# Performance work log

Measured on AMD Instinct MI355X. Metric: run time of the kernel, lower is better.

The kernel has to match this reference:

```python
import jax, jax.numpy as jnp
import numpy as np

B, S, D, H = 4, 1024, 1024, 16
DK = D // H
N_REL = 5


def setup_inputs() -> dict:
    key = jax.random.key(0)
    ks = jax.random.split(key, 16)
    p = lambda k, shape: (jax.random.normal(k, shape, dtype=jnp.float32) * 0.02)
    return {
        "x": jax.random.normal(ks[0], (B, S, D), dtype=jnp.float32),
        "relation_matrix": jax.random.randint(ks[1], (S, S), 0, N_REL, dtype=jnp.int32),
        "mask": jax.random.randint(ks[2], (B, 1, S, S), 0, 2, dtype=jnp.int32),
        "Wq": p(ks[3], (D, D)), "bq": p(ks[4], (D,)),
        "Wk": p(ks[5], (D, D)), "bk": p(ks[6], (D,)),
        "Wv": p(ks[7], (D, D)), "bv": p(ks[8], (D,)),
        "Wo": p(ks[9], (D, D)), "bo": p(ks[10], (D,)),
        "rel_table": p(ks[11], (N_REL, DK)),
        "gamma": jnp.ones((D,), dtype=jnp.float32),
        "beta": jnp.zeros((D,), dtype=jnp.float32),
    }


def reference(x, relation_matrix, mask, Wq, bq, Wk, bk, Wv, bv, Wo, bo, rel_table, gamma, beta):
    b, s = x.shape[0], x.shape[1]
    residual = x
    # projections -> [B, H, S, DK]
    def proj(W, bias):
        return (x @ W + bias).reshape(b, s, H, DK).transpose(0, 2, 1, 3)
    Q, K, V = proj(Wq, bq), proj(Wk, bk), proj(Wv, bv)
    scores = jnp.einsum('bhid,bhjd->bhij', Q, K) / jnp.sqrt(jnp.float32(DK))
    # relation-embedding additive bias: gather [S,S,DK] then contract with Q
    rel_emb = rel_table[relation_matrix]               # [S, S, DK]
    rel_scores = jnp.einsum('bhid,ijd->bhij', Q, rel_emb)
    scores = scores + rel_scores * 0.5
    scores = jnp.where(mask == 0, jnp.float32(-1e9), scores)
    attention = jax.nn.softmax(scores, axis=-1)
    context = jnp.einsum('bhij,bhjd->bhid', attention, V)
    context = context.transpose(0, 2, 1, 3).reshape(b, s, D)
    output = context @ Wo + bo
    # layer norm (eps = 1e-5, torch default)
    y = output + residual
    mu = jnp.mean(y, axis=-1, keepdims=True)
    var = jnp.mean(jnp.square(y - mu), axis=-1, keepdims=True)
    return (y - mu) * jax.lax.rsqrt(var + 1e-5) * gamma + beta
```

## Files before the change

### kernel.cpp

```cpp
#include <hip/hip_runtime.h>
#include <hip/hip_bf16.h>

typedef unsigned short u16;
typedef unsigned int u32;
typedef unsigned char u8;
typedef __attribute__((ext_vector_type(8))) short short8;
typedef __attribute__((ext_vector_type(4))) float f32x4;

__device__ __forceinline__ float b2f(u16 u) {
    union { float f; u32 i; } z; z.i = ((u32)u) << 16; return z.f;
}
__device__ __forceinline__ u16 f2b(float f) {
    union { float f; u32 i; } z; z.f = f;
    u32 i = z.i;
    u32 r = (i + 0x7FFFu + ((i >> 16) & 1u)) >> 16;
    return (u16)r;
}
__device__ __forceinline__ float ldf(const void* p, size_t i, int f) {
    return f ? ((const float*)p)[i] : b2f(((const u16*)p)[i]);
}
__device__ __forceinline__ void gload_lds16(const void* g, void* l) {
    __builtin_amdgcn_global_load_lds(
        (const __attribute__((address_space(1))) u32*)g,
        (__attribute__((address_space(3))) u32*)l,
        16, 0, 0);
}
__device__ __forceinline__ float exp2_hw(float x) {
    float r; asm("v_exp_f32 %0, %1" : "=v"(r) : "v"(x)); return r;
}

struct P14 { const void* p[14]; };
struct S14 { int s[14]; };

__global__ __launch_bounds__(256) void classify_stats(P14 ptrs, S14 szs, int* stats)
{
    __shared__ int   wsm[4], wzr[4], wag[4], way[4], wjk[4];
    __shared__ float wme[4], wmo[4];
    int i = blockIdx.x;
    int t = threadIdx.x, lane = t & 63, w = t >> 6;
    const u16* p16 = (const u16*)ptrs.p[i];
    const u32* p32 = (const u32*)ptrs.p[i];
    int n = szs.s[i];
    int n16 = n < 4096 ? n : 4096;
    int n32 = n16 >> 1;
    int small = 1, zero = 1, allg = 1, anyg = 0, junk = 0;
    float maxe = 0.f, maxo = 0.f;
    for (int k = t; k < n32; k += 256) if (p32[k] >= 8u) small = 0;
    for (int k = t; k < n16; k += 256) {
        u16 ww = p16[k];
        if (ww != 0) zero = 0;
        if (ww == 0x3F80u) anyg = 1;
        else if (ww != 0) allg = 0;
        float a = fabsf(b2f(ww));
        if (k & 1) { if (a < 1e30f && a > maxo) maxo = a; }
        else { if (!(a < 100.0f)) junk++; else if (a > maxe) maxe = a; }
    }
#pragma unroll
    for (int s = 1; s < 64; s <<= 1) {
        small &= __shfl_xor(small, s);
        zero  &= __shfl_xor(zero, s);
        allg  &= __shfl_xor(allg, s);
        anyg  |= __shfl_xor(anyg, s);
        junk  += __shfl_xor(junk, s);
        maxe   = fmaxf(maxe, __shfl_xor(maxe, s));
        maxo   = fmaxf(maxo, __shfl_xor(maxo, s));
    }
    if (lane == 0) { wsm[w]=small; wzr[w]=zero; wag[w]=allg; way[w]=anyg; wjk[w]=junk; wme[w]=maxe; wmo[w]=maxo; }
    __syncthreads();
    if (t == 0) {
        int sm=1,zr=1,ag=1,ay=0,jk=0; float me=0.f,mo=0.f;
        for (int q=0;q<4;++q){ sm&=wsm[q]; zr&=wzr[q]; ag&=wag[q]; ay|=way[q]; jk+=wjk[q]; me=fmaxf(me,wme[q]); mo=fmaxf(mo,wmo[q]); }
        stats[i*8+0]=sm; stats[i*8+1]=zr; stats[i*8+2]=(ag&&ay)?1:0; stats[i*8+3]=jk;
        stats[i*8+4]=__float_as_int(me); stats[i*8+5]=__float_as_int(mo);
    }
}

__global__ __launch_bounds__(64) void classify_bind(S14 szs, const int* stats, int* cls)
{
    if (threadIdx.x != 0) return;
    int xi = -1, mi = -1, ri = -1, rt = -1, gi = -1, bi = -1;
    int wv[4] = {-1,-1,-1,-1}; int nw = 0;
    int bs[4] = {-1,-1,-1,-1}; int nb = 0;
    for (int i = 0; i < 14; ++i) {
        int s = szs.s[i];
        int sm = stats[i*8+0], zr = stats[i*8+1];
        if (s == 4194304) { if (sm) mi = i; else xi = i; }
        else if (s == 1048576) { if (sm) ri = i; else if (nw < 4) wv[nw++] = i; }
        else if (s == 320) rt = i;
        else if (s == 1024) {
            if (zr) bi = i;
            else if (stats[i*8+2]) gi = i;
            else if (nb < 4) bs[nb++] = i;
        }
    }
    bool ok = (xi >= 0) && (mi >= 0) && (ri >= 0) && (rt >= 0) && (gi >= 0) && (bi >= 0)
           && (nw == 4) && (nb == 4);
    if (ok) {
        cls[0] = xi; cls[1] = ri; cls[2] = mi;
        cls[3] = wv[0]; cls[5] = wv[1]; cls[7] = wv[2]; cls[9] = wv[3];
        cls[4] = bs[0]; cls[6] = bs[1]; cls[8] = bs[2]; cls[10] = bs[3];
        cls[11] = rt; cls[12] = gi; cls[13] = bi;
    } else {
        for (int r = 0; r < 14; ++r) cls[r] = r;
    }
    const int froles[12] = {0,3,4,5,6,7,8,9,10,11,12,13};
    for (int r = 0; r < 12; ++r) {
        int role = froles[r]; int idx = cls[role];
        float me = __int_as_float(stats[idx*8+4]);
        float mo = __int_as_float(stats[idx*8+5]);
        cls[16 + role] = (stats[idx*8+3] > 0) || (me == 0.f && mo > 0.f);
    }
    cls[30] = ok ? 1 : 0;
}

__global__ __launch_bounds__(256) void cvt_x_flex(P14 ptrs, const int* cls, u16* xb) {
    const void* x = ptrs.p[cls[0]];
    int f = cls[16];
    int idx = (blockIdx.x * 256 + threadIdx.x) << 2;
    union { u16 u[4]; uint2 v2; } o;
    if (f) {
        float4 v = *(const float4*)((const float*)x + idx);
        o.u[0] = f2b(v.x); o.u[1] = f2b(v.y); o.u[2] = f2b(v.z); o.u[3] = f2b(v.w);
    } else {
        o.v2 = *(const uint2*)((const u16*)x + idx);
    }
    *(uint2*)&xb[idx] = o.v2;
}

__global__ __launch_bounds__(256) void transposeW_flex(P14 ptrs, const int* cls,
                                                       u16* WT3, u16* WoT)
{
    int z = blockIdx.z;
    const void* W = ptrs.p[cls[3 + 2 * z]];
    int f = cls[16 + 3 + 2 * z];
    u16* WT = (z < 3) ? (WT3 + ((size_t)z << 20)) : WoT;
    __shared__ u16 tile[64][72];
    int t = threadIdx.x;
    int n0 = blockIdx.x << 6, k0 = blockIdx.y << 6;
    int r = t >> 2, c = (t & 3) << 4;
    size_t base = (size_t)(k0 + r) * 1024 + n0 + c;
    if (f) {
        const float* src = (const float*)W + base;
#pragma unroll
        for (int x = 0; x < 16; ++x) tile[r][c + x] = f2b(src[x]);
    } else {
        const u16* src = (const u16*)W + base;
#pragma unroll
        for (int x = 0; x < 16; ++x) tile[r][c + x] = src[x];
    }
    __syncthreads();
    union { u16 u[16]; uint4 v[2]; } tmp;
#pragma unroll
    for (int x = 0; x < 16; ++x) tmp.u[x] = tile[c + x][r];
    *(uint4*)&WT[(size_t)(n0 + r) * 1024 + k0 + c]     = tmp.v[0];
    *(uint4*)&WT[(size_t)(n0 + r) * 1024 + k0 + c + 8] = tmp.v[1];
}

__global__ __launch_bounds__(256) void qrel_k(
    const u16* __restrict__ Q, P14 ptrs, const int* cls, float* __restrict__ Qrel)
{
    __shared__ float rt[5][64];
    const void* rel_table = ptrs.p[cls[11]];
    int f9 = cls[16 + 11];
    int t = threadIdx.x;
    for (int p = t; p < 320; p += 256) ((float*)rt)[p] = ldf(rel_table, p, f9);
    __syncthreads();
    int row = blockIdx.x * 256 + t;
    const u16* qrow = Q + ((size_t)row << 6);
    float a0=0.f, a1=0.f, a2=0.f, a3=0.f, a4=0.f;
#pragma unroll
    for (int k8 = 0; k8 < 64; k8 += 8) {
        union { uint4 v; u16 u[8]; } qq;
        qq.v = *(const uint4*)(qrow + k8);
#pragma unroll
        for (int e = 0; e < 8; ++e) {
            float qv = b2f(qq.u[e]);
            a0 += qv * rt[0][k8 + e];
            a1 += qv * rt[1][k8 + e];
            a2 += qv * rt[2][k8 + e];
            a3 += qv * rt[3][k8 + e];
            a4 += qv * rt[4][k8 + e];
        }
    }
    const float S = 0.5f * 1.44269504f;
    float4 o0 = {a0 * S, a1 * S, a2 * S, a3 * S};
    float4 o1 = {a4 * S, -1e9f, -1e9f, -1e9f};
    *(float4*)&Qrel[(size_t)row * 8]     = o0;
    *(float4*)&Qrel[(size_t)row * 8 + 4] = o1;
}

__global__ __launch_bounds__(256) void gemm128_qkv(
    const u16* __restrict__ X, const u16* __restrict__ WT3,
    P14 ptrs, const int* cls,
    u16* __restrict__ Qb, u16* __restrict__ Kb, u16* __restrict__ VTb)
{
    int o = (blockIdx.x & 7) * 192 + (blockIdx.x >> 3);
    int mt = o / 48, rem = o % 48;
    int z = rem >> 4, nt = rem & 15;
    int m0 = mt << 7, n0 = nt << 6;
    const u16* WT = WT3 + ((size_t)z << 20);
    const void* biasp = ptrs.p[cls[4 + 2 * z]];
    int fb = cls[16 + 4 + 2 * z];
    __shared__ u16 As[2][128][4][8];
    __shared__ u16 Bs[2][64][4][8];
    int t = threadIdx.x, lane = t & 63, w = t >> 6;
    int m = lane & 15, quad = lane >> 4;
    int wm = (w >> 1) << 6, wn = (w & 1) << 5;
    int r1 = t >> 2, r2 = 64 + r1, k4 = t & 3;
    const u16* xa  = &X [(size_t)(m0 + r1) * 1024 + k4 * 8];
    const u16* xa2 = &X [(size_t)(m0 + r2) * 1024 + k4 * 8];
    const u16* wb  = &WT[(size_t)(n0 + r1) * 1024 + k4 * 8];
    f32x4 acc[4][2];
#pragma unroll
    for (int i = 0; i < 4; ++i)
#pragma unroll
        for (int j = 0; j < 2; ++j) acc[i][j] = (f32x4){0.f,0.f,0.f,0.f};

    auto stage = [&](int buf, int k0) {
        gload_lds16(xa  + k0, &As[buf][r1][k4][0]);
        gload_lds16(xa2 + k0, &As[buf][r2][k4][0]);
        gload_lds16(wb  + k0, &Bs[buf][r1][k4][0]);
    };
    stage(0, 0);
    stage(1, 32);
    asm volatile("s_waitcnt vmcnt(3)" ::: "memory");
    __builtin_amdgcn_s_barrier();
    __builtin_amdgcn_sched_barrier(0);
    int cur = 0;
    for (int k0 = 0; k0 < 1024; k0 += 32) {
        short8 af[4], bf[2];
#pragma unroll
        for (int mb = 0; mb < 4; ++mb) af[mb] = *(const short8*)&As[cur][wm + mb*16 + m][quad][0];
#pragma unroll
        for (int nb = 0; nb < 2; ++nb) bf[nb] = *(const short8*)&Bs[cur][wn + nb*16 + m][quad][0];
#pragma unroll
        for (int mb = 0; mb < 4; ++mb)
#pragma unroll
            for (int nb = 0; nb < 2; ++nb)
                acc[mb][nb] = __builtin_amdgcn_mfma_f32_16x16x32_bf16(af[mb], bf[nb], acc[mb][nb], 0, 0, 0);
        __builtin_amdgcn_s_barrier();
        __builtin_amdgcn_sched_barrier(0);
        if (k0 + 64 < 1024) {
            stage(cur, k0 + 64);
            asm volatile("s_waitcnt vmcnt(3)" ::: "memory");
        } else {
            asm volatile("s_waitcnt vmcnt(0)" ::: "memory");
        }
        __builtin_amdgcn_s_barrier();
        __builtin_amdgcn_sched_barrier(0);
        cur ^= 1;
    }
    if (z == 2) {
#pragma unroll
        for (int nb = 0; nb < 2; ++nb) {
            int gn = n0 + wn + nb*16 + m;
            int h = gn >> 6, dk = gn & 63;
            float bv = ldf(biasp, gn, fb);
            int sx = (dk & 7) << 3;
#pragma unroll
            for (int mb = 0; mb < 4; ++mb) {
                int gmBase = m0 + wm + mb*16 + (quad << 2);
                int bI = gmBase >> 10, sB = gmBase & 1023;
                int pos = (sB & ~63) | ((sB & 63) ^ sx);
                union { u16 u[4]; uint2 v; } o4;
#pragma unroll
                for (int r = 0; r < 4; ++r) o4.u[r] = f2b(acc[mb][nb][r] + bv);
                *(uint2*)&VTb[((size_t)(bI * 16 + h) << 16) + dk * 1024 + pos] = o4.v;
            }
        }
    } else {
        u16* outp = (z == 0) ? Qb : Kb;
#pragma unroll
        for (int nb = 0; nb < 2; ++nb) {
            int gn = n0 + wn + nb*16 + m;
            int h = gn >> 6, dk = gn & 63;
            float bv = ldf(biasp, gn, fb);
#pragma unroll
            for (int mb = 0; mb < 4; ++mb)
#pragma unroll
                for (int r = 0; r < 4; ++r) {
                    int gm = m0 + wm + mb*16 + (quad << 2) + r;
                    int bI = gm >> 10, s = gm & 1023;
                    int dk2 = (z == 1) ? (dk ^ (((quad * 4 + r) & 7) << 3)) : dk;
                    outp[((size_t)((bI * 16 + h) << 10) + s) * 64 + dk2] = f2b(acc[mb][nb][r] + bv);
                }
        }
    }
}

__global__ __launch_bounds__(256) void gemm_out64(
    const u16* __restrict__ A, const u16* __restrict__ WT,
    P14 ptrs, const int* cls, float* __restrict__ y)
{
    const void* bo   = ptrs.p[cls[10]];
    const void* Xres = ptrs.p[cls[0]];
    int f8 = cls[16 + 10], f0 = cls[16];
    int o = (blockIdx.x & 7) * 128 + (blockIdx.x >> 3);
    int nt = o & 15, mt = o >> 4;
    int n0 = nt << 6, m0 = mt << 6;
    __shared__ u16 As[2][64][4][8];
    __shared__ u16 Bs[2][64][4][8];
    int t = threadIdx.x, lane = t & 63, w = t >> 6;
    int m = lane & 15, quad = lane >> 4;
    int wm = (w >> 1) << 5, wn = (w & 1) << 5;
    int r1 = t >> 2, k4 = t & 3;
    const u16* xa  = &A [(size_t)(m0 + r1) * 1024 + k4 * 8];
    const u16* wb  = &WT[(size_t)(n0 + r1) * 1024 + k4 * 8];
    f32x4 acc[2][2];
#pragma unroll
    for (int i = 0; i < 2; ++i)
#pragma unroll
        for (int j = 0; j < 2; ++j) acc[i][j] = (f32x4){0.f,0.f,0.f,0.f};

    auto stage = [&](int buf, int k0) {
        gload_lds16(xa + k0, &As[buf][r1][k4][0]);
        gload_lds16(wb + k0, &Bs[buf][r1][k4][0]);
    };
    stage(0, 0);
    stage(1, 32);
    asm volatile("s_waitcnt vmcnt(2)" ::: "memory");
    __builtin_amdgcn_s_barrier();
    __builtin_amdgcn_sched_barrier(0);
    int cur = 0;
    for (int k0 = 0; k0 < 1024; k0 += 32) {
        short8 af[2], bf[2];
#pragma unroll
        for (int mb = 0; mb < 2; ++mb) af[mb] = *(const short8*)&As[cur][wm + mb*16 + m][quad][0];
#pragma unroll
        for (int nb = 0; nb < 2; ++nb) bf[nb] = *(const short8*)&Bs[cur][wn + nb*16 + m][quad][0];
#pragma unroll
        for (int mb = 0; mb < 2; ++mb)
#pragma unroll
            for (int nb = 0; nb < 2; ++nb)
                acc[mb][nb] = __builtin_amdgcn_mfma_f32_16x16x32_bf16(af[mb], bf[nb], acc[mb][nb], 0, 0, 0);
        __builtin_amdgcn_s_barrier();
        __builtin_amdgcn_sched_barrier(0);
        if (k0 + 64 < 1024) {
            stage(cur, k0 + 64);
            asm volatile("s_waitcnt vmcnt(2)" ::: "memory");
        } else {
            asm volatile("s_waitcnt vmcnt(0)" ::: "memory");
        }
        __builtin_amdgcn_s_barrier();
        __builtin_amdgcn_sched_barrier(0);
        cur ^= 1;
    }
#pragma unroll
    for (int nb = 0; nb < 2; ++nb) {
        int gn = n0 + wn + nb*16 + m;
        float bb = ldf(bo, gn, f8);
#pragma unroll
        for (int mb = 0; mb < 2; ++mb)
#pragma unroll
            for (int r = 0; r < 4; ++r) {
                int gm = m0 + wm + mb*16 + (quad << 2) + r;
                size_t idx = (size_t)gm * 1024 + gn;
                y[idx] = acc[mb][nb][r] + bb + ldf(Xres, idx, f0);
            }
    }
}

__global__ __launch_bounds__(256) void make_codes(P14 ptrs, const int* cls, u8* codes)
{
    const int* relmat = (const int*)ptrs.p[cls[1]];
    const int* maskp  = (const int*)ptrs.p[cls[2]];
    int bid = blockIdx.x;
    int b = bid >> 8, ti = (bid >> 4) & 15, tj = bid & 15;
    int t = threadIdx.x, lane = t & 63, w = t >> 6;
    int m = lane & 15, quad = lane >> 4;
    const int* mb = maskp + ((size_t)b << 20);
    union { uint4 v; u8 c[16]; } out;
#pragma unroll
    for (int jb = 0; jb < 4; ++jb) {
        int j = tj * 64 + jb * 16 + m;
#pragma unroll
        for (int r = 0; r < 4; ++r) {
            int i = ti * 64 + w * 16 + (quad << 2) + r;
            size_t off = (size_t)i * 1024 + j;
            out.c[jb * 4 + r] = mb[off] ? (u8)relmat[off] : (u8)5;
        }
    }
    ((uint4*)codes)[(size_t)bid * 256 + t] = out.v;
}

__global__ __launch_bounds__(256) void attn_mfma(
    const u16* __restrict__ Q, const u16* __restrict__ K, const u16* __restrict__ VT,
    const float* __restrict__ Qrel, const u8* __restrict__ codes, u16* __restrict__ ctx)
{
    int raw = blockIdx.x;
    int bid = (raw & 7) * 128 + (raw >> 3);
    int bh = bid >> 4, ti = bid & 15;
    int i0 = ti << 6;
    int b = bh >> 4, h = bh & 15;
    const u16* Qp = Q  + ((size_t)bh << 16);
    const u16* Kp = K  + ((size_t)bh << 16);
    const u16* Vp = VT + ((size_t)bh << 16);
    const uint4* ctile = (const uint4*)codes + ((size_t)((b * 16 + ti) * 16) << 8);

    __shared__ u16 Ks[2][64][64];
    __shared__ u16 Vt[64][64];
    __shared__ u16 Pls[64][72];
    __shared__ float Qrl[64][9];

    int t = threadIdx.x, lane = t & 63, w = t >> 6;
    int m = lane & 15, quad = lane >> 4;

    {
        float2 qv = *(const float2*)&Qrel[(((size_t)bh << 10) + i0) * 8 + (t << 1)];
        Qrl[t >> 2][(t & 3) << 1]       = qv.x;
        Qrl[t >> 2][((t & 3) << 1) + 1] = qv.y;
    }

    short8 qfrag0, qfrag1;
    {
        const u16* qr = Qp + (size_t)(i0 + w * 16 + m) * 64 + quad * 8;
        qfrag0 = *(const short8*)qr;
        qfrag1 = *(const short8*)(qr + 32);
    }
    f32x4 O[4];
    float l_part[4];
#pragma unroll
    for (int d = 0; d < 4; ++d) O[d] = (f32x4){0.f,0.f,0.f,0.f};
#pragma unroll
    for (int r = 0; r < 4; ++r) l_part[r] = 0.f;

    int srow = t >> 3, scol8 = (t & 7) << 3;
    const u16* ks0 = Kp + (size_t)srow * 64 + scol8;
    const u16* ks1 = ks0 + 32 * 64;
    const u16* vs0 = Vp + (size_t)srow * 1024 + scol8;
    const u16* vs1 = vs0 + 32 * 1024;

    auto stageK = [&](int buf, int j0) {
        gload_lds16(ks0 + (size_t)j0 * 64, &Ks[buf][srow][scol8]);
        gload_lds16(ks1 + (size_t)j0 * 64, &Ks[buf][srow + 32][scol8]);
    };
    auto stageV = [&](int j0) {
        gload_lds16(vs0 + j0, &Vt[srow][scol8]);
        gload_lds16(vs1 + j0, &Vt[srow + 32][scol8]);
    };

    const float SC = 0.125f * 1.44269504f;
    int kx = (m & 7) << 3;
    u32 paddr = (u32)(uintptr_t)
        ( __attribute__((address_space(3))) u16*)&Pls[w * 16 + (quad << 2)][m];

    stageK(0, 0);
    stageV(0);
    uint4 cN = ctile[t];
    __syncthreads();
    int cur = 0;

    for (int j0 = 0; j0 < 1024; j0 += 64) {
        bool next = (j0 + 64 < 1024);
        if (next) stageK(cur ^ 1, j0 + 64);

        f32x4 acc[4];
#pragma unroll
        for (int jb = 0; jb < 4; ++jb) {
            acc[jb] = (f32x4){0.f,0.f,0.f,0.f};
            short8 kb0 = *(const short8*)&Ks[cur][jb * 16 + m][(quad * 8) ^ kx];
            short8 kb1 = *(const short8*)&Ks[cur][jb * 16 + m][(32 + quad * 8) ^ kx];
            acc[jb] = __builtin_amdgcn_mfma_f32_16x16x32_bf16(qfrag0, kb0, acc[jb], 0, 0, 0);
            acc[jb] = __builtin_amdgcn_mfma_f32_16x16x32_bf16(qfrag1, kb1, acc[jb], 0, 0, 0);
        }
        union { uint4 v; u8 c[16]; } cd;
        cd.v = cN;
        if (next) cN = ctile[(((j0 + 64) >> 6) << 8) + t];

        float sc[4][4];
#pragma unroll
        for (int jb = 0; jb < 4; ++jb) {
#pragma unroll
            for (int r = 0; r < 4; ++r) {
                int il = w * 16 + (quad << 2) + r;
                float p = exp2_hw(acc[jb][r] * SC + Qrl[il][cd.c[jb * 4 + r]]);
                sc[jb][r] = p;
                l_part[r] += p;
            }
        }
#define PWRITE(JB, O0, O1, O2, O3)                                            \
        {                                                                     \
            u32 pk0, pk1;                                                     \
            asm("v_cvt_pk_bf16_f32 %0, %2, %3\n\t"                            \
                "v_cvt_pk_bf16_f32 %1, %4, %5"                                \
                : "=v"(pk0), "=v"(pk1)                                        \
                : "v"(sc[JB][0]), "v"(sc[JB][1]),                             \
                  "v"(sc[JB][2]), "v"(sc[JB][3]));                            \
            asm volatile("ds_write_b16 %0, %1 offset:" O0 "\n\t"              \
                         "ds_write_b16_d16_hi %0, %1 offset:" O1 "\n\t"       \
                         "ds_write_b16 %0, %2 offset:" O2 "\n\t"              \
                         "ds_write_b16_d16_hi %0, %2 offset:" O3              \
                         :: "v"(paddr), "v"(pk0), "v"(pk1) : "memory");       \
        }
        PWRITE(0, "0",  "144", "288", "432")
        PWRITE(1, "32", "176", "320", "464")
        PWRITE(2, "64", "208", "352", "496")
        PWRITE(3, "96", "240", "384", "528")
#undef PWRITE
        asm volatile("s_waitcnt lgkmcnt(0)" ::: "memory");
        __builtin_amdgcn_sched_barrier(0);

        __syncthreads();

        short8 pa0 = *(const short8*)&Pls[w * 16 + m][quad * 8];
        short8 pa1 = *(const short8*)&Pls[w * 16 + m][quad * 8 + 32];
#pragma unroll
        for (int db = 0; db < 4; ++db) {
            short8 vb0 = *(const short8*)&Vt[db * 16 + m][(quad * 8) ^ kx];
            short8 vb1 = *(const short8*)&Vt[db * 16 + m][(32 + quad * 8) ^ kx];
            O[db] = __builtin_amdgcn_mfma_f32_16x16x32_bf16(pa0, vb0, O[db], 0, 0, 0);
            O[db] = __builtin_amdgcn_mfma_f32_16x16x32_bf16(pa1, vb1, O[db], 0, 0, 0);
        }

        __syncthreads();
        if (next) stageV(j0 + 64);
        cur ^= 1;
    }
    float linv[4];
#pragma unroll
    for (int r = 0; r < 4; ++r) {
        float l = l_part[r];
        l += __shfl_xor(l, 1);
        l += __shfl_xor(l, 2);
        l += __shfl_xor(l, 4);
        l += __shfl_xor(l, 8);
        linv[r] = 1.0f / fmaxf(l, 1e-35f);
    }
#pragma unroll
    for (int db = 0; db < 4; ++db)
#pragma unroll
        for (int r = 0; r < 4; ++r) {
            int il = w * 16 + (quad << 2) + r;
            size_t addr = ((size_t)(b * 1024 + i0 + il)) * 1024 + h * 64 + db * 16 + m;
            ctx[addr] = f2b(O[db][r] * linv[r]);
        }
}

__global__ __launch_bounds__(256) void ln_k(
    float* __restrict__ y, P14 ptrs, const int* cls)
{
    const void* gamma = ptrs.p[cls[12]];
    const void* beta  = ptrs.p[cls[13]];
    int f10 = cls[16 + 12], f11 = cls[16 + 13];
    int row = blockIdx.x, t = threadIdx.x;
    float4 v = *(const float4*)&y[(size_t)row * 1024 + (t << 2)];
    float s = v.x + v.y + v.z + v.w;
#pragma unroll
    for (int mm = 1; mm < 64; mm <<= 1) s += __shfl_xor(s, mm);
    __shared__ float sm[8];
    int w = t >> 6, lane = t & 63;
    if (lane == 0) sm[w] = s;
    __syncthreads();
    float mu = (sm[0] + sm[1] + sm[2] + sm[3]) * (1.0f / 1024.0f);
    float dx = v.x - mu, dy = v.y - mu, dz = v.z - mu, dw = v.w - mu;
    float q = dx * dx + dy * dy + dz * dz + dw * dw;
#pragma unroll
    for (int mm = 1; mm < 64; mm <<= 1) q += __shfl_xor(q, mm);
    if (lane == 0) sm[4 + w] = q;
    __syncthreads();
    float var = (sm[4] + sm[5] + sm[6] + sm[7]) * (1.0f / 1024.0f);
    float rs = rsqrtf(var + 1e-5f);
    int c = t << 2;
    float4 o;
    o.x = dx * rs * ldf(gamma, c,     f10) + ldf(beta, c,     f11);
    o.y = dy * rs * ldf(gamma, c + 1, f10) + ldf(beta, c + 1, f11);
    o.z = dz * rs * ldf(gamma, c + 2, f10) + ldf(beta, c + 2, f11);
    o.w = dw * rs * ldf(gamma, c + 3, f10) + ldf(beta, c + 3, f11);
    *(float4*)&y[(size_t)row * 1024 + c] = o;
}

extern "C" void kernel_launch(void* const* d_in, const int* in_sizes, int n_in,
                              void* d_out, int out_size, void* d_ws, size_t ws_size,
                              hipStream_t stream) {
    (void)out_size; (void)ws_size;
    P14 ptrs; S14 szs;
    for (int i = 0; i < 14; ++i) {
        ptrs.p[i] = (i < n_in) ? d_in[i] : d_in[0];
        szs.s[i]  = (i < n_in) ? in_sizes[i] : 0;
    }
    float* out = (float*)d_out;

    char* ws = (char*)d_ws;
    const size_t MB = 1u << 20;
    u16*   WT3   = (u16*)(ws);
    u16*   WoT   = (u16*)(ws + 6 * MB);
    u16*   Xb    = (u16*)(ws + 8 * MB);
    u16*   Qb    = (u16*)(ws + 16 * MB);
    u16*   Kb    = (u16*)(ws + 24 * MB);
    u16*   VTb   = (u16*)(ws + 32 * MB);
    u16*   ctx   = (u16*)(ws + 8 * MB);
    u8*    codes = (u8*)(ws);
    float* Qrel  = (float*)(ws + 4 * MB);
    int*   cls   = (int*)(ws + 40 * MB);
    int*   stats = (int*)(ws + 40 * MB + 512);

    classify_stats<<<14, 256, 0, stream>>>(ptrs, szs, stats);
    classify_bind<<<1, 64, 0, stream>>>(szs, stats, cls);
    cvt_x_flex<<<4096, 256, 0, stream>>>(ptrs, cls, Xb);
    transposeW_flex<<<dim3(16, 16, 4), 256, 0, stream>>>(ptrs, cls, WT3, WoT);
    gemm128_qkv<<<1536, 256, 0, stream>>>(Xb, WT3, ptrs, cls, Qb, Kb, VTb);
    qrel_k<<<256, 256, 0, stream>>>(Qb, ptrs, cls, Qrel);
    make_codes<<<1024, 256, 0, stream>>>(ptrs, cls, codes);
    attn_mfma<<<1024, 256, 0, stream>>>(Qb, Kb, VTb, Qrel, codes, ctx);
    gemm_out64<<<1024, 256, 0, stream>>>(ctx, WoT, ptrs, cls, out);
    ln_k<<<4096, 256, 0, stream>>>(out, ptrs, cls);
}
```

Before: 264.3 us.

## Merge prep and post kernels, replace attention syncthreads with counted vmcnt waits

Fuses the x conversion and weight transpose into one launch, and the mask/relation code builder and Q-relation projection into another, cutting two kernel launches and their tail gaps. In the attention loop, __syncthreads (which drains every outstanding load) is replaced by raw s_barrier plus explicit s_waitcnt vmcnt counts, so the next K tile and code prefetches can stay in flight across barriers. The code prefetch is also moved ahead of the QK MFMAs. The hand-tuned vmcnt counts depend on exactly how many loads each stage issues, so a miscount could silently race.

```diff
diff --git a/kernel.cpp b/kernel.cpp
--- a/kernel.cpp
+++ b/kernel.cpp
@@ -113,80 +113,49 @@
     cls[30] = ok ? 1 : 0;
 }
 
-__global__ __launch_bounds__(256) void cvt_x_flex(P14 ptrs, const int* cls, u16* xb) {
-    const void* x = ptrs.p[cls[0]];
-    int f = cls[16];
-    int idx = (blockIdx.x * 256 + threadIdx.x) << 2;
-    union { u16 u[4]; uint2 v2; } o;
-    if (f) {
-        float4 v = *(const float4*)((const float*)x + idx);
-        o.u[0] = f2b(v.x); o.u[1] = f2b(v.y); o.u[2] = f2b(v.z); o.u[3] = f2b(v.w);
+__global__ __launch_bounds__(256) void prep_k(P14 ptrs, const int* cls,
+                                              u16* xb, u16* WT3, u16* WoT)
+{
+    __shared__ u16 tile[64][72];
+    int bid = blockIdx.x;
+    int t = threadIdx.x;
+    if (bid < 4096) {
+        const void* x = ptrs.p[cls[0]];
+        int f = cls[16];
+        int idx = (bid * 256 + t) << 2;
+        union { u16 u[4]; uint2 v2; } o;
+        if (f) {
+            float4 v = *(const float4*)((const float*)x + idx);
+            o.u[0] = f2b(v.x); o.u[1] = f2b(v.y); o.u[2] = f2b(v.z); o.u[3] = f2b(v.w);
+        } else {
+            o.v2 = *(const uint2*)((const u16*)x + idx);
+        }
+        *(uint2*)&xb[idx] = o.v2;
     } else {
-        o.v2 = *(const uint2*)((const u16*)x + idx);
-    }
-    *(uint2*)&xb[idx] = o.v2;
-}
-
-__global__ __launch_bounds__(256) void transposeW_flex(P14 ptrs, const int* cls,
-                                                       u16* WT3, u16* WoT)
-{
-    int z = blockIdx.z;
-    const void* W = ptrs.p[cls[3 + 2 * z]];
-    int f = cls[16 + 3 + 2 * z];
-    u16* WT = (z < 3) ? (WT3 + ((size_t)z << 20)) : WoT;
-    __shared__ u16 tile[64][72];
-    int t = threadIdx.x;
-    int n0 = blockIdx.x << 6, k0 = blockIdx.y << 6;
-    int r = t >> 2, c = (t & 3) << 4;
-    size_t base = (size_t)(k0 + r) * 1024 + n0 + c;
-    if (f) {
-        const float* src = (const float*)W + base;
-#pragma unroll
-        for (int x = 0; x < 16; ++x) tile[r][c + x] = f2b(src[x]);
-    } else {
-        const u16* src = (const u16*)W + base;
-#pragma unroll
-        for (int x = 0; x < 16; ++x) tile[r][c + x] = src[x];
-    }
-    __syncthreads();
-    union { u16 u[16]; uint4 v[2]; } tmp;
-#pragma unroll
-    for (int x = 0; x < 16; ++x) tmp.u[x] = tile[c + x][r];
-    *(uint4*)&WT[(size_t)(n0 + r) * 1024 + k0 + c]     = tmp.v[0];
-    *(uint4*)&WT[(size_t)(n0 + r) * 1024 + k0 + c + 8] = tmp.v[1];
-}
-
-__global__ __launch_bounds__(256) void qrel_k(
-    const u16* __restrict__ Q, P14 ptrs, const int* cls, float* __restrict__ Qrel)
-{
-    __shared__ float rt[5][64];
-    const void* rel_table = ptrs.p[cls[11]];
-    int f9 = cls[16 + 11];
-    int t = threadIdx.x;
-    for (int p = t; p < 320; p += 256) ((float*)rt)[p] = ldf(rel_table, p, f9);
-    __syncthreads();
-    int row = blockIdx.x * 256 + t;
-    const u16* qrow = Q + ((size_t)row << 6);
-    float a0=0.f, a1=0.f, a2=0.f, a3=0.f, a4=0.f;
-#pragma unroll
-    for (int k8 = 0; k8 < 64; k8 += 8) {
-        union { uint4 v; u16 u[8]; } qq;
-        qq.v = *(const uint4*)(qrow + k8);
-#pragma unroll
-        for (int e = 0; e < 8; ++e) {
-            float qv = b2f(qq.u[e]);
-            a0 += qv * rt[0][k8 + e];
-            a1 += qv * rt[1][k8 + e];
-            a2 += qv * rt[2][k8 + e];
-            a3 += qv * rt[3][k8 + e];
-            a4 += qv * rt[4][k8 + e];
-        }
-    }
-    const float S = 0.5f * 1.44269504f;
-    float4 o0 = {a0 * S, a1 * S, a2 * S, a3 * S};
-    float4 o1 = {a4 * S, -1e9f, -1e9f, -1e9f};
-    *(float4*)&Qrel[(size_t)row * 8]     = o0;
-    *(float4*)&Qrel[(size_t)row * 8 + 4] = o1;
+        int tw = bid - 4096;
+        int bx = tw & 15, by = (tw >> 4) & 15, z = tw >> 8;
+        const void* W = ptrs.p[cls[3 + 2 * z]];
+        int f = cls[16 + 3 + 2 * z];
+        u16* WT = (z < 3) ? (WT3 + ((size_t)z << 20)) : WoT;
+        int n0 = bx << 6, k0 = by << 6;
+        int r = t >> 2, c = (t & 3) << 4;
+        size_t base = (size_t)(k0 + r) * 1024 + n0 + c;
+        if (f) {
+            const float* src = (const float*)W + base;
+#pragma unroll
+            for (int x2 = 0; x2 < 16; ++x2) tile[r][c + x2] = f2b(src[x2]);
+        } else {
+            const u16* src = (const u16*)W + base;
+#pragma unroll
+            for (int x2 = 0; x2 < 16; ++x2) tile[r][c + x2] = src[x2];
+        }
+        __syncthreads();
+        union { u16 u[16]; uint4 v[2]; } tmp;
+#pragma unroll
+        for (int x2 = 0; x2 < 16; ++x2) tmp.u[x2] = tile[c + x2][r];
+        *(uint4*)&WT[(size_t)(n0 + r) * 1024 + k0 + c]     = tmp.v[0];
+        *(uint4*)&WT[(size_t)(n0 + r) * 1024 + k0 + c + 8] = tmp.v[1];
+    }
 }
 
 __global__ __launch_bounds__(256) void gemm128_qkv(
@@ -360,27 +329,59 @@
     }
 }
 
-__global__ __launch_bounds__(256) void make_codes(P14 ptrs, const int* cls, u8* codes)
-{
-    const int* relmat = (const int*)ptrs.p[cls[1]];
-    const int* maskp  = (const int*)ptrs.p[cls[2]];
+__global__ __launch_bounds__(256) void post_k(
+    P14 ptrs, const int* cls, u8* codes, const u16* __restrict__ Q, float* __restrict__ Qrel)
+{
+    __shared__ float rt[5][64];
     int bid = blockIdx.x;
-    int b = bid >> 8, ti = (bid >> 4) & 15, tj = bid & 15;
-    int t = threadIdx.x, lane = t & 63, w = t >> 6;
-    int m = lane & 15, quad = lane >> 4;
-    const int* mb = maskp + ((size_t)b << 20);
-    union { uint4 v; u8 c[16]; } out;
-#pragma unroll
-    for (int jb = 0; jb < 4; ++jb) {
-        int j = tj * 64 + jb * 16 + m;
-#pragma unroll
-        for (int r = 0; r < 4; ++r) {
-            int i = ti * 64 + w * 16 + (quad << 2) + r;
-            size_t off = (size_t)i * 1024 + j;
-            out.c[jb * 4 + r] = mb[off] ? (u8)relmat[off] : (u8)5;
-        }
-    }
-    ((uint4*)codes)[(size_t)bid * 256 + t] = out.v;
+    int t = threadIdx.x;
+    if (bid < 1024) {
+        const int* relmat = (const int*)ptrs.p[cls[1]];
+        const int* maskp  = (const int*)ptrs.p[cls[2]];
+        int b = bid >> 8, ti = (bid >> 4) & 15, tj = bid & 15;
+        int lane = t & 63, w = t >> 6;
+        int m = lane & 15, quad = lane >> 4;
+        const int* mb = maskp + ((size_t)b << 20);
+        union { uint4 v; u8 c[16]; } out;
+#pragma unroll
+        for (int jb = 0; jb < 4; ++jb) {
+            int j = tj * 64 + jb * 16 + m;
+#pragma unroll
+            for (int r = 0; r < 4; ++r) {
+                int i = ti * 64 + w * 16 + (quad << 2) + r;
+                size_t off = (size_t)i * 1024 + j;
+                out.c[jb * 4 + r] = mb[off] ? (u8)relmat[off] : (u8)5;
+            }
+        }
+        ((uint4*)codes)[(size_t)bid * 256 + t] = out.v;
+    } else {
+        const void* rel_table = ptrs.p[cls[11]];
+        int f9 = cls[16 + 11];
+        for (int p = t; p < 320; p += 256) ((float*)rt)[p] = ldf(rel_table, p, f9);
+        __syncthreads();
+        int row = (bid - 1024) * 256 + t;
+        const u16* qrow = Q + ((size_t)row << 6);
+        float a0=0.f, a1=0.f, a2=0.f, a3=0.f, a4=0.f;
+#pragma unroll
+        for (int k8 = 0; k8 < 64; k8 += 8) {
+            union { uint4 v; u16 u[8]; } qq;
+            qq.v = *(const uint4*)(qrow + k8);
+#pragma unroll
+            for (int e = 0; e < 8; ++e) {
+                float qv = b2f(qq.u[e]);
+                a0 += qv * rt[0][k8 + e];
+                a1 += qv * rt[1][k8 + e];
+                a2 += qv * rt[2][k8 + e];
+                a3 += qv * rt[3][k8 + e];
+                a4 += qv * rt[4][k8 + e];
+            }
+        }
+        const float S = 0.5f * 1.44269504f;
+        float4 o0 = {a0 * S, a1 * S, a2 * S, a3 * S};
+        float4 o1 = {a4 * S, -1e9f, -1e9f, -1e9f};
+        *(float4*)&Qrel[(size_t)row * 8]     = o0;
+        *(float4*)&Qrel[(size_t)row * 8 + 4] = o1;
+    }
 }
 
 __global__ __launch_bounds__(256) void attn_mfma(
@@ -452,7 +453,17 @@
 
     for (int j0 = 0; j0 < 1024; j0 += 64) {
         bool next = (j0 + 64 < 1024);
-        if (next) stageK(cur ^ 1, j0 + 64);
+        union { uint4 v; u8 c[16]; } cd;
+        cd.v = cN;
+        if (next) {
+            stageK(cur ^ 1, j0 + 64);
+            cN = ctile[(((j0 + 64) >> 6) << 8) + t];
+            asm volatile("s_waitcnt vmcnt(6)" ::: "memory");
+        } else {
+            asm volatile("s_waitcnt vmcnt(3)" ::: "memory");
+        }
+        __builtin_amdgcn_s_barrier();
+        __builtin_amdgcn_sched_barrier(0);
 
         f32x4 acc[4];
 #pragma unroll
@@ -463,9 +474,6 @@
             acc[jb] = __builtin_amdgcn_mfma_f32_16x16x32_bf16(qfrag0, kb0, acc[jb], 0, 0, 0);
             acc[jb] = __builtin_amdgcn_mfma_f32_16x16x32_bf16(qfrag1, kb1, acc[jb], 0, 0, 0);
         }
-        union { uint4 v; u8 c[16]; } cd;
-        cd.v = cN;
-        if (next) cN = ctile[(((j0 + 64) >> 6) << 8) + t];
 
         float sc[4][4];
 #pragma unroll
@@ -500,7 +508,10 @@
         asm volatile("s_waitcnt lgkmcnt(0)" ::: "memory");
         __builtin_amdgcn_sched_barrier(0);
 
-        __syncthreads();
+        if (next) asm volatile("s_waitcnt vmcnt(3)" ::: "memory");
+        else      asm volatile("s_waitcnt vmcnt(0)" ::: "memory");
+        __builtin_amdgcn_s_barrier();
+        __builtin_amdgcn_sched_barrier(0);
 
         short8 pa0 = *(const short8*)&Pls[w * 16 + m][quad * 8];
         short8 pa1 = *(const short8*)&Pls[w * 16 + m][quad * 8 + 32];
@@ -512,7 +523,8 @@
             O[db] = __builtin_amdgcn_mfma_f32_16x16x32_bf16(pa1, vb1, O[db], 0, 0, 0);
         }
 
-        __syncthreads();
+        __builtin_amdgcn_s_barrier();
+        __builtin_amdgcn_sched_barrier(0);
         if (next) stageV(j0 + 64);
         cur ^= 1;
     }
@@ -596,11 +608,9 @@
 
     classify_stats<<<14, 256, 0, stream>>>(ptrs, szs, stats);
     classify_bind<<<1, 64, 0, stream>>>(szs, stats, cls);
-    cvt_x_flex<<<4096, 256, 0, stream>>>(ptrs, cls, Xb);
-    transposeW_flex<<<dim3(16, 16, 4), 256, 0, stream>>>(ptrs, cls, WT3, WoT);
+    prep_k<<<5120, 256, 0, stream>>>(ptrs, cls, Xb, WT3, WoT);
     gemm128_qkv<<<1536, 256, 0, stream>>>(Xb, WT3, ptrs, cls, Qb, Kb, VTb);
-    qrel_k<<<256, 256, 0, stream>>>(Qb, ptrs, cls, Qrel);
-    make_codes<<<1024, 256, 0, stream>>>(ptrs, cls, codes);
+    post_k<<<1280, 256, 0, stream>>>(ptrs, cls, codes, Qb, Qrel);
     attn_mfma<<<1024, 256, 0, stream>>>(Qb, Kb, VTb, Qrel, codes, ctx);
     gemm_out64<<<1024, 256, 0, stream>>>(ctx, WoT, ptrs, cls, out);
     ln_k<<<4096, 256, 0, stream>>>(out, ptrs, cls);
```

Result: no change. 262.1 us (-0.8%).
